# Kernel tuning notes

Hardware: AMD Instinct MI355X
Metric: run time of the kernel (lower is better)

Reference implementation:

```python
import jax, jax.numpy as jnp
import numpy as np

B, S, E, H = 4, 1024, 1024, 16
HD = E // H


def setup_inputs() -> dict:
    key = jax.random.key(0)
    ks = jax.random.split(key, 5)
    x = jax.random.normal(ks[0], (B, S, E), dtype=jnp.float32)
    # causal mask: True = masked (filled with -inf), as in masked_fill_
    mask = jnp.triu(jnp.ones((S, S), dtype=bool), k=1)
    in_proj_weight = jax.random.normal(ks[1], (3 * E, E), dtype=jnp.float32) * (E ** -0.5)
    in_proj_bias = jax.random.normal(ks[2], (3 * E,), dtype=jnp.float32) * 0.02
    out_w = jax.random.normal(ks[3], (E, E), dtype=jnp.float32) * (E ** -0.5)
    out_b = jax.random.normal(ks[4], (E,), dtype=jnp.float32) * 0.02
    return {"x": x, "mask": mask, "in_proj_weight": in_proj_weight,
            "in_proj_bias": in_proj_bias, "out_w": out_w, "out_b": out_b}


def reference(x, mask, in_proj_weight, in_proj_bias, out_w, out_b):
    scaling = HD ** -0.5
    # fused QKV projection (self-attention path: qkv_same)
    qkv = jnp.einsum('bse,fe->bsf', x, in_proj_weight) + in_proj_bias  # [B,S,3E]
    q, k, v = jnp.split(qkv, 3, axis=-1)
    # split heads -> [B,H,S,HD]
    def heads(t):
        return t.reshape(B, S, H, HD).transpose(0, 2, 1, 3)
    q, k, v = heads(q), heads(k), heads(v)
    scores = jnp.einsum('bhsd,bhtd->bhst', q, k) * scaling  # [B,H,S,S]
    scores = jnp.where(mask[None, None, :, :], -jnp.inf, scores)
    att = jax.nn.softmax(scores, axis=-1)  # dropout p=0.0 (eval)
    out = jnp.einsum('bhst,bhtd->bhsd', att, v)  # [B,H,S,HD]
    out = out.transpose(0, 2, 1, 3).reshape(B, S, E)  # concat heads
    out = jnp.einsum('bse,fe->bsf', out, out_w) + out_b
    att_weights = att.reshape(B * H, S, S)
    return out, att_weights
```

## Files before the change

kernel.cpp:

```cpp
#include <hip/hip_runtime.h>
#include <hip/hip_bf16.h>
#include <stdint.h>

#define NH 16
#define SEQ 1024
#define EMB 1024
#define HDIM 64
#define BATCH 4
#define SPAD 1032

typedef float f32x4 __attribute__((ext_vector_type(4)));
typedef short bf16x8 __attribute__((ext_vector_type(8)));

static __device__ __forceinline__ short f2bf(float f) {
  union { float f; uint32_t u; } v; v.f = f;
  uint32_t r = (v.u + 0x7FFF + ((v.u >> 16) & 1)) >> 16;
  return (short)(uint16_t)r;
}
static __device__ __forceinline__ float bf2f(short h) {
  union { uint32_t u; float f; } v; v.u = ((uint32_t)(uint16_t)h) << 16;
  return v.f;
}

static __device__ __forceinline__ void gload_lds16(const void* g, void* l) {
  __builtin_amdgcn_global_load_lds(
      (const __attribute__((address_space(1))) void*)g,
      (__attribute__((address_space(3))) void*)l, 16, 0, 0);
}

static __device__ __forceinline__ void cvt8(const float* s, short* d) {
  const float4* sv = (const float4*)s;
  float4 a = sv[0], b = sv[1];
  bf16x8 o;
  o[0] = f2bf(a.x); o[1] = f2bf(a.y); o[2] = f2bf(a.z); o[3] = f2bf(a.w);
  o[4] = f2bf(b.x); o[5] = f2bf(b.y); o[6] = f2bf(b.z); o[7] = f2bf(b.w);
  *(bf16x8*)d = o;
}

__global__ void cvt3_kernel(const float* __restrict__ x, const float* __restrict__ w,
                            const float* __restrict__ o, short* __restrict__ xb,
                            short* __restrict__ wb, short* __restrict__ ob) {
  int i = (blockIdx.x * blockDim.x + threadIdx.x) * 8;
  if (i < 4194304) {
    cvt8(x + i, xb + i);
  } else if (i < 7340032) {
    cvt8(w + (i - 4194304), wb + (i - 4194304));
  } else {
    cvt8(o + (i - 7340032), ob + (i - 7340032));
  }
}

__global__ __launch_bounds__(256) void transpose_v(const short* __restrict__ v,
                                                   short* __restrict__ vt) {
  __shared__ short t[64][72];
  const int tid = threadIdx.x;
  const int bh = blockIdx.y;
  const int sb = blockIdx.x * 64;
  const int row = tid >> 2;
  const int c0 = (tid & 3) * 16;
  const short* src = v + ((size_t)(bh * SEQ + sb + row)) * HDIM + c0;
  *(bf16x8*)&t[row][c0] = *(const bf16x8*)src;
  *(bf16x8*)&t[row][c0 + 8] = *(const bf16x8*)(src + 8);
  __syncthreads();
  bf16x8 o0, o1;
#pragma unroll
  for (int i = 0; i < 8; ++i) o0[i] = t[c0 + i][row];
#pragma unroll
  for (int i = 0; i < 8; ++i) o1[i] = t[c0 + 8 + i][row];
  short* dst = vt + ((size_t)(bh * HDIM + row)) * SEQ + sb + c0;
  *(bf16x8*)dst = o0;
  *(bf16x8*)(dst + 8) = o1;
}

__global__ __launch_bounds__(256) void gemm_qkv(
    const short* __restrict__ A, const short* __restrict__ Bm,
    const float* __restrict__ bias, short* __restrict__ qkvws) {
  __shared__ short As[128 * 64];
  __shared__ short Bs[128 * 64];
  const int tid = threadIdx.x;
  const int w = tid >> 6, l = tid & 63;
  const int l15 = l & 15, l4 = l >> 4;
  const int wr = w >> 1, wc = w & 1;
  const int row0 = blockIdx.x * 128;
  const int col0 = blockIdx.y * 128;
  const int K = EMB;

  f32x4 acc[4][4] = {};

  const int o = (w * 4) * 1024 + l * 16;
  for (int k0 = 0; k0 < K; k0 += 64) {
#pragma unroll
    for (int c = 0; c < 4; ++c) {
      int oo = o + c * 1024;
      int row = oo >> 7;
      int colb = oo & 127;
      int scol = colb ^ ((row & 7) << 4);
      gload_lds16((const char*)A + ((size_t)(row0 + row) * K + k0) * 2 + scol,
                  (char*)As + (w * 4 + c) * 1024);
      gload_lds16((const char*)Bm + ((size_t)(col0 + row) * K + k0) * 2 + scol,
                  (char*)Bs + (w * 4 + c) * 1024);
    }
    __syncthreads();
#pragma unroll
    for (int kk = 0; kk < 2; ++kk) {
      bf16x8 af[4], bfr[4];
      const int kb = (kk * 64 + l4 * 16) ^ ((l15 & 7) << 4);
#pragma unroll
      for (int i = 0; i < 4; ++i) {
        af[i] = *(const bf16x8*)((const char*)As + (wr * 64 + i * 16 + l15) * 128 + kb);
        bfr[i] = *(const bf16x8*)((const char*)Bs + (wc * 64 + i * 16 + l15) * 128 + kb);
      }
#pragma unroll
      for (int i = 0; i < 4; ++i)
#pragma unroll
        for (int j = 0; j < 4; ++j)
          acc[i][j] = __builtin_amdgcn_mfma_f32_16x16x32_bf16(af[i], bfr[j], acc[i][j], 0, 0, 0);
    }
    __syncthreads();
  }

#pragma unroll
  for (int j = 0; j < 4; ++j) {
    int f = col0 + wc * 64 + j * 16 + l15;
    float bv = bias[f];
    int part = f >> 10;
    int e = f & 1023;
    int hh = e >> 6, d = e & 63;
#pragma unroll
    for (int i = 0; i < 4; ++i) {
#pragma unroll
      for (int rr = 0; rr < 4; ++rr) {
        int m = row0 + wr * 64 + i * 16 + l4 * 4 + rr;
        int bb = m >> 10, ss = m & 1023;
        qkvws[(size_t)part * 4194304 +
              ((size_t)(bb * NH + hh) * SEQ + ss) * HDIM + d] =
            f2bf(acc[i][j][rr] + bv);
      }
    }
  }
}

__global__ __launch_bounds__(256) void gemm_out64(
    const short* __restrict__ A, const short* __restrict__ Bm,
    const float* __restrict__ bias, float* __restrict__ outp) {
  __shared__ short As[128 * 64];
  __shared__ short Bs[64 * 64];
  const int tid = threadIdx.x;
  const int w = tid >> 6, l = tid & 63;
  const int l15 = l & 15, l4 = l >> 4;
  const int row0 = blockIdx.x * 128;
  const int col0 = blockIdx.y * 64;
  const int K = EMB;

  f32x4 acc[2][4] = {};

  const int oA = (w * 4) * 1024 + l * 16;
  const int oB = (w * 2) * 1024 + l * 16;
  for (int k0 = 0; k0 < K; k0 += 64) {
#pragma unroll
    for (int c = 0; c < 4; ++c) {
      int oo = oA + c * 1024;
      int row = oo >> 7;
      int colb = oo & 127;
      int scol = colb ^ ((row & 7) << 4);
      gload_lds16((const char*)A + ((size_t)(row0 + row) * K + k0) * 2 + scol,
                  (char*)As + (w * 4 + c) * 1024);
    }
#pragma unroll
    for (int c = 0; c < 2; ++c) {
      int oo = oB + c * 1024;
      int row = oo >> 7;
      int colb = oo & 127;
      int scol = colb ^ ((row & 7) << 4);
      gload_lds16((const char*)Bm + ((size_t)(col0 + row) * K + k0) * 2 + scol,
                  (char*)Bs + (w * 2 + c) * 1024);
    }
    __syncthreads();
#pragma unroll
    for (int kk = 0; kk < 2; ++kk) {
      bf16x8 af[2], bfr[4];
      const int kb = (kk * 64 + l4 * 16) ^ ((l15 & 7) << 4);
#pragma unroll
      for (int i = 0; i < 2; ++i)
        af[i] = *(const bf16x8*)((const char*)As + (w * 32 + i * 16 + l15) * 128 + kb);
#pragma unroll
      for (int j = 0; j < 4; ++j)
        bfr[j] = *(const bf16x8*)((const char*)Bs + (j * 16 + l15) * 128 + kb);
#pragma unroll
      for (int i = 0; i < 2; ++i)
#pragma unroll
        for (int j = 0; j < 4; ++j)
          acc[i][j] = __builtin_amdgcn_mfma_f32_16x16x32_bf16(af[i], bfr[j], acc[i][j], 0, 0, 0);
    }
    __syncthreads();
  }

#pragma unroll
  for (int j = 0; j < 4; ++j) {
    int f = col0 + j * 16 + l15;
    float bv = bias[f];
#pragma unroll
    for (int i = 0; i < 2; ++i)
#pragma unroll
      for (int rr = 0; rr < 4; ++rr) {
        int m = row0 + w * 32 + i * 16 + l4 * 4 + rr;
        __builtin_nontemporal_store(acc[i][j][rr] + bv, &outp[(size_t)m * EMB + f]);
      }
  }
}

__global__ __launch_bounds__(256) void attn_kernel(
    const short* __restrict__ qws, const short* __restrict__ kws,
    const short* __restrict__ vtws, float* __restrict__ attg,
    short* __restrict__ aow) {
  __shared__ short strip[32 * SPAD];
  __shared__ float wsum[4][32];
  __shared__ float inv_sum[32];

  const int tid = threadIdx.x;
  const int w = tid >> 6, l = tid & 63;
  const int l15 = l & 15, l4 = l >> 4;
  const int blk = blockIdx.x;
  const int bh = blk >> 5;
  const int r = blk & 31;
  const int rowbase = r * 32;

  const short* qb = qws + ((size_t)bh * SEQ + rowbase) * HDIM;
  const short* kb = kws + (size_t)bh * SEQ * HDIM;
  const short* vb = vtws + (size_t)bh * HDIM * SEQ;

  bf16x8 qf[2][2];
#pragma unroll
  for (int rg = 0; rg < 2; ++rg)
#pragma unroll
    for (int ks = 0; ks < 2; ++ks)
      qf[rg][ks] = *(const bf16x8*)(qb + (rg * 16 + l15) * HDIM + ks * 32 + l4 * 8);

  const int ngroups = (rowbase + 32) >> 4;
  float psum[2][4] = {};

  for (int g = w; g < ngroups; g += 4) {
    const short* kg = kb + (g * 16 + l15) * HDIM + l4 * 8;
    bf16x8 kf0 = *(const bf16x8*)(kg);
    bf16x8 kf1 = *(const bf16x8*)(kg + 32);
    f32x4 a0 = {}, a1 = {};
    a0 = __builtin_amdgcn_mfma_f32_16x16x32_bf16(qf[0][0], kf0, a0, 0, 0, 0);
    a0 = __builtin_amdgcn_mfma_f32_16x16x32_bf16(qf[0][1], kf1, a0, 0, 0, 0);
    a1 = __builtin_amdgcn_mfma_f32_16x16x32_bf16(qf[1][0], kf0, a1, 0, 0, 0);
    a1 = __builtin_amdgcn_mfma_f32_16x16x32_bf16(qf[1][1], kf1, a1, 0, 0, 0);
    int col = g * 16 + l15;
#pragma unroll
    for (int rg = 0; rg < 2; ++rg) {
#pragma unroll
      for (int rr = 0; rr < 4; ++rr) {
        int rloc = rg * 16 + l4 * 4 + rr;
        int row = rowbase + rloc;
        float sv = (rg ? a1[rr] : a0[rr]) * 0.125f;
        float ev = (col <= row) ? __expf(sv) : 0.0f;
        psum[rg][rr] += ev;
        strip[rloc * SPAD + col] = f2bf(ev);
      }
    }
  }

#pragma unroll
  for (int rg = 0; rg < 2; ++rg)
#pragma unroll
    for (int rr = 0; rr < 4; ++rr) {
      float v = psum[rg][rr];
      v += __shfl_xor(v, 1);
      v += __shfl_xor(v, 2);
      v += __shfl_xor(v, 4);
      v += __shfl_xor(v, 8);
      psum[rg][rr] = v;
    }
  if (l15 == 0) {
#pragma unroll
    for (int rg = 0; rg < 2; ++rg)
#pragma unroll
      for (int rr = 0; rr < 4; ++rr)
        wsum[w][rg * 16 + l4 * 4 + rr] = psum[rg][rr];
  }
  __syncthreads();
  if (tid < 32) {
    float s = wsum[0][tid] + wsum[1][tid] + wsum[2][tid] + wsum[3][tid];
    inv_sum[tid] = 1.0f / s;
  }
  __syncthreads();

  {
    const int limit = ngroups * 16;
    const int rloc = tid >> 3;
    const int cb = tid & 7;
    float* arow = attg + (size_t)bh * SEQ * SEQ + (size_t)(rowbase + rloc) * SEQ;
    float isr = inv_sum[rloc];
#pragma unroll
    for (int i = 0; i < 16; ++i) {
      int c = (cb + i * 8) * 8;
      f32x4 o0, o1;
      if (c < limit) {
        bf16x8 p = *(const bf16x8*)&strip[rloc * SPAD + c];
        o0[0] = bf2f(p[0]) * isr; o0[1] = bf2f(p[1]) * isr;
        o0[2] = bf2f(p[2]) * isr; o0[3] = bf2f(p[3]) * isr;
        o1[0] = bf2f(p[4]) * isr; o1[1] = bf2f(p[5]) * isr;
        o1[2] = bf2f(p[6]) * isr; o1[3] = bf2f(p[7]) * isr;
      } else {
        o0 = (f32x4)0.0f;
        o1 = (f32x4)0.0f;
      }
      __builtin_nontemporal_store(o0, (f32x4*)(arow + c));
      __builtin_nontemporal_store(o1, (f32x4*)(arow + c + 4));
    }
  }

  {
    const int nch = ngroups >> 1;
    const int d0 = w * 16;
    f32x4 oacc[2] = {};
    const short* vrow = vb + (d0 + l15) * SEQ + l4 * 8;
    for (int c = 0; c < nch; ++c) {
      bf16x8 vf = *(const bf16x8*)(vrow + c * 32);
      bf16x8 p0 = *(const bf16x8*)&strip[(0 + l15) * SPAD + c * 32 + l4 * 8];
      bf16x8 p1 = *(const bf16x8*)&strip[(16 + l15) * SPAD + c * 32 + l4 * 8];
      oacc[0] = __builtin_amdgcn_mfma_f32_16x16x32_bf16(p0, vf, oacc[0], 0, 0, 0);
      oacc[1] = __builtin_amdgcn_mfma_f32_16x16x32_bf16(p1, vf, oacc[1], 0, 0, 0);
    }
    const int b = bh >> 4, h = bh & 15;
#pragma unroll
    for (int rg = 0; rg < 2; ++rg) {
#pragma unroll
      for (int rr = 0; rr < 4; ++rr) {
        int rloc = rg * 16 + l4 * 4 + rr;
        int s = rowbase + rloc;
        float v = oacc[rg][rr] * inv_sum[rloc];
        aow[((size_t)(b * SEQ + s)) * EMB + h * HDIM + d0 + l15] = f2bf(v);
      }
    }
  }
}

extern "C" void kernel_launch(void* const* d_in, const int* in_sizes, int n_in,
                              void* d_out, int out_size, void* d_ws, size_t ws_size,
                              hipStream_t stream) {
  (void)in_sizes; (void)n_in; (void)out_size; (void)ws_size;
  const float* x = (const float*)d_in[0];
  const float* ipw = (const float*)d_in[2];
  const float* ipb = (const float*)d_in[3];
  const float* ow = (const float*)d_in[4];
  const float* ob = (const float*)d_in[5];
  float* outp = (float*)d_out;
  float* attg = (float*)d_out + (size_t)BATCH * SEQ * EMB;

  char* ws = (char*)d_ws;
  short* xbf = (short*)(ws);
  short* wbf = (short*)(ws + 8388608);
  short* owbf = (short*)(ws + 14680064);
  short* qkvws = (short*)(ws + 16777216);
  short* aow = (short*)(ws + 41943040);
  short* vtws = (short*)(ws);

  short* qws = qkvws;
  short* kws = qkvws + 4194304;
  short* vws = qkvws + 8388608;

  cvt3_kernel<<<4096, 256, 0, stream>>>(x, ipw, ow, xbf, wbf, owbf);

  dim3 g1(32, 24);
  gemm_qkv<<<g1, 256, 0, stream>>>(xbf, wbf, ipb, qkvws);

  transpose_v<<<dim3(16, 64), 256, 0, stream>>>(vws, vtws);

  attn_kernel<<<2048, 256, 0, stream>>>(qws, kws, vtws, attg, aow);

  gemm_out64<<<dim3(32, 16), 256, 0, stream>>>(aow, owbf, ob, outp);
}
```

Before: 184.6 us.

## Double-buffer LDS tiles in QKV and output projection GEMMs

Both projection GEMMs now use two LDS buffers for the A and B tiles. The next k-tile's global-to-LDS load is issued before the MFMA work on the current tile, so loads overlap compute instead of waiting behind a barrier each step. This doubles LDS use per block, to 64KB for the QKV GEMM and 48KB for the output GEMM, which can lower occupancy. The async LDS loads may also need correct waitcnt handling before the next barrier.

```diff
diff --git a/kernel.cpp b/kernel.cpp
--- a/kernel.cpp
+++ b/kernel.cpp
@@ -72,11 +72,24 @@
   *(bf16x8*)(dst + 8) = o1;
 }
 
+#define STAGE_QKV(bb, kk0)                                                     \
+  {                                                                            \
+    _Pragma("unroll") for (int c = 0; c < 4; ++c) {                            \
+      int oo = o + c * 1024;                                                   \
+      int row = oo >> 7;                                                       \
+      int scol = (oo & 127) ^ ((row & 7) << 4);                                \
+      gload_lds16((const char*)A + ((size_t)(row0 + row) * K + (kk0)) * 2 + scol, \
+                  (char*)As[bb] + (w * 4 + c) * 1024);                         \
+      gload_lds16((const char*)Bm + ((size_t)(col0 + row) * K + (kk0)) * 2 + scol,\
+                  (char*)Bs[bb] + (w * 4 + c) * 1024);                         \
+    }                                                                          \
+  }
+
 __global__ __launch_bounds__(256) void gemm_qkv(
     const short* __restrict__ A, const short* __restrict__ Bm,
     const float* __restrict__ bias, short* __restrict__ qkvws) {
-  __shared__ short As[128 * 64];
-  __shared__ short Bs[128 * 64];
+  __shared__ short As[2][128 * 64];
+  __shared__ short Bs[2][128 * 64];
   const int tid = threadIdx.x;
   const int w = tid >> 6, l = tid & 63;
   const int l15 = l & 15, l4 = l >> 4;
@@ -88,27 +101,20 @@
   f32x4 acc[4][4] = {};
 
   const int o = (w * 4) * 1024 + l * 16;
+  STAGE_QKV(0, 0);
+  __syncthreads();
+
+  int cur = 0;
   for (int k0 = 0; k0 < K; k0 += 64) {
-#pragma unroll
-    for (int c = 0; c < 4; ++c) {
-      int oo = o + c * 1024;
-      int row = oo >> 7;
-      int colb = oo & 127;
-      int scol = colb ^ ((row & 7) << 4);
-      gload_lds16((const char*)A + ((size_t)(row0 + row) * K + k0) * 2 + scol,
-                  (char*)As + (w * 4 + c) * 1024);
-      gload_lds16((const char*)Bm + ((size_t)(col0 + row) * K + k0) * 2 + scol,
-                  (char*)Bs + (w * 4 + c) * 1024);
-    }
-    __syncthreads();
+    if (k0 + 64 < K) STAGE_QKV(cur ^ 1, k0 + 64);
 #pragma unroll
     for (int kk = 0; kk < 2; ++kk) {
       bf16x8 af[4], bfr[4];
       const int kb = (kk * 64 + l4 * 16) ^ ((l15 & 7) << 4);
 #pragma unroll
       for (int i = 0; i < 4; ++i) {
-        af[i] = *(const bf16x8*)((const char*)As + (wr * 64 + i * 16 + l15) * 128 + kb);
-        bfr[i] = *(const bf16x8*)((const char*)Bs + (wc * 64 + i * 16 + l15) * 128 + kb);
+        af[i] = *(const bf16x8*)((const char*)As[cur] + (wr * 64 + i * 16 + l15) * 128 + kb);
+        bfr[i] = *(const bf16x8*)((const char*)Bs[cur] + (wc * 64 + i * 16 + l15) * 128 + kb);
       }
 #pragma unroll
       for (int i = 0; i < 4; ++i)
@@ -117,6 +123,7 @@
           acc[i][j] = __builtin_amdgcn_mfma_f32_16x16x32_bf16(af[i], bfr[j], acc[i][j], 0, 0, 0);
     }
     __syncthreads();
+    cur ^= 1;
   }
 
 #pragma unroll
@@ -140,11 +147,29 @@
   }
 }
 
+#define STAGE_OUT(bb, kk0)                                                     \
+  {                                                                            \
+    _Pragma("unroll") for (int c = 0; c < 4; ++c) {                            \
+      int oo = oA + c * 1024;                                                  \
+      int row = oo >> 7;                                                       \
+      int scol = (oo & 127) ^ ((row & 7) << 4);                                \
+      gload_lds16((const char*)A + ((size_t)(row0 + row) * K + (kk0)) * 2 + scol, \
+                  (char*)As[bb] + (w * 4 + c) * 1024);                         \
+    }                                                                          \
+    _Pragma("unroll") for (int c = 0; c < 2; ++c) {                            \
+      int oo = oB + c * 1024;                                                  \
+      int row = oo >> 7;                                                       \
+      int scol = (oo & 127) ^ ((row & 7) << 4);                                \
+      gload_lds16((const char*)Bm + ((size_t)(col0 + row) * K + (kk0)) * 2 + scol,\
+                  (char*)Bs[bb] + (w * 2 + c) * 1024);                         \
+    }                                                                          \
+  }
+
 __global__ __launch_bounds__(256) void gemm_out64(
     const short* __restrict__ A, const short* __restrict__ Bm,
     const float* __restrict__ bias, float* __restrict__ outp) {
-  __shared__ short As[128 * 64];
-  __shared__ short Bs[64 * 64];
+  __shared__ short As[2][128 * 64];
+  __shared__ short Bs[2][64 * 64];
   const int tid = threadIdx.x;
   const int w = tid >> 6, l = tid & 63;
   const int l15 = l & 15, l4 = l >> 4;
@@ -156,36 +181,22 @@
 
   const int oA = (w * 4) * 1024 + l * 16;
   const int oB = (w * 2) * 1024 + l * 16;
+  STAGE_OUT(0, 0);
+  __syncthreads();
+
+  int cur = 0;
   for (int k0 = 0; k0 < K; k0 += 64) {
-#pragma unroll
-    for (int c = 0; c < 4; ++c) {
-      int oo = oA + c * 1024;
-      int row = oo >> 7;
-      int colb = oo & 127;
-      int scol = colb ^ ((row & 7) << 4);
-      gload_lds16((const char*)A + ((size_t)(row0 + row) * K + k0) * 2 + scol,
-                  (char*)As + (w * 4 + c) * 1024);
-    }
-#pragma unroll
-    for (int c = 0; c < 2; ++c) {
-      int oo = oB + c * 1024;
-      int row = oo >> 7;
-      int colb = oo & 127;
-      int scol = colb ^ ((row & 7) << 4);
-      gload_lds16((const char*)Bm + ((size_t)(col0 + row) * K + k0) * 2 + scol,
-                  (char*)Bs + (w * 2 + c) * 1024);
-    }
-    __syncthreads();
+    if (k0 + 64 < K) STAGE_OUT(cur ^ 1, k0 + 64);
 #pragma unroll
     for (int kk = 0; kk < 2; ++kk) {
       bf16x8 af[2], bfr[4];
       const int kb = (kk * 64 + l4 * 16) ^ ((l15 & 7) << 4);
 #pragma unroll
       for (int i = 0; i < 2; ++i)
-        af[i] = *(const bf16x8*)((const char*)As + (w * 32 + i * 16 + l15) * 128 + kb);
+        af[i] = *(const bf16x8*)((const char*)As[cur] + (w * 32 + i * 16 + l15) * 128 + kb);
 #pragma unroll
       for (int j = 0; j < 4; ++j)
-        bfr[j] = *(const bf16x8*)((const char*)Bs + (j * 16 + l15) * 128 + kb);
+        bfr[j] = *(const bf16x8*)((const char*)Bs[cur] + (j * 16 + l15) * 128 + kb);
 #pragma unroll
       for (int i = 0; i < 2; ++i)
 #pragma unroll
@@ -193,6 +204,7 @@
           acc[i][j] = __builtin_amdgcn_mfma_f32_16x16x32_bf16(af[i], bfr[j], acc[i][j], 0, 0, 0);
     }
     __syncthreads();
+    cur ^= 1;
   }
 
 #pragma unroll
```

Result: faster. 177.0 us (-4.1%).
